# Performance work log

Measured on AMD Instinct MI355X. Metric: run time of the kernel, lower is better.

The kernel has to match this reference:

```python
import jax, jax.numpy as jnp
import numpy as np

B, S = 4, 2048            # batch, seq_len
IN, OUT, NQ = 4096, 4096, 3  # in_features, out_features, num quant levels


def setup_inputs() -> dict:
    key = jax.random.key(0)
    kx, ka = jax.random.split(key, 2)
    x = jax.random.normal(kx, (B, S, IN), dtype=jnp.float32)
    # init_alpha: log(uniform distribution) + tiny noise
    alpha = jnp.log(jnp.full((OUT, IN, NQ), 1.0 / NQ, dtype=jnp.float32)) \
        + 1e-5 * (jax.random.uniform(ka, (OUT, IN, NQ), dtype=jnp.float32) - 0.5)
    quant_vals = jnp.array([-1.0, 0.0, 1.0], dtype=jnp.float32)
    bias = jnp.zeros((OUT,), dtype=jnp.float32)
    return {"x": x, "alpha": alpha, "quant_vals": quant_vals, "bias": bias}


def reference(x, alpha, quant_vals, bias):
    # sample_softmax with temp=1, random=1, hard=False (module globals)
    # gumbels = -log(Exp(1)) == standard Gumbel noise
    g = jax.random.gumbel(jax.random.key(42), alpha.shape, dtype=alpha.dtype)
    y_soft = jax.nn.softmax(alpha + g, axis=-1)          # [OUT, IN, NQ]
    weight = jnp.einsum('oiq,q->oi', y_soft, quant_vals)  # dense dequantized weight
    # F.linear(x, weight, bias) = x @ weight.T + bias
    return jnp.einsum('bsi,oi->bso', x, weight) + bias
```

## Files before the change

### kernel.cpp

```cpp
#include <hip/hip_runtime.h>
#include <hip/hip_fp16.h>
#include <stdint.h>


#define PRNG_PARTITIONABLE 1

#define OUT_F 4096
#define IN_F  4096
#define MROWS 8192
#define NQV   3

typedef __attribute__((ext_vector_type(4))) _Float16 f16x4;
typedef __attribute__((ext_vector_type(8))) _Float16 f16x8;
typedef __attribute__((ext_vector_type(4))) float    f32x4;

__device__ __forceinline__ uint32_t rotl32(uint32_t x, int r) {
  return (x << r) | (x >> (32 - r));
}

__device__ __forceinline__ void threefry2x32(uint32_t x0, uint32_t x1,
                                             uint32_t& o0, uint32_t& o1) {
  const uint32_t ks0 = 0u, ks1 = 42u;
  const uint32_t ks2 = ks0 ^ ks1 ^ 0x1BD11BDAu;
  x0 += ks0; x1 += ks1;
#define TF_R(r) { x0 += x1; x1 = rotl32(x1, r); x1 ^= x0; }
  TF_R(13) TF_R(15) TF_R(26) TF_R(6)
  x0 += ks1; x1 += ks2 + 1u;
  TF_R(17) TF_R(29) TF_R(16) TF_R(24)
  x0 += ks2; x1 += ks0 + 2u;
  TF_R(13) TF_R(15) TF_R(26) TF_R(6)
  x0 += ks0; x1 += ks1 + 3u;
  TF_R(17) TF_R(29) TF_R(16) TF_R(24)
  x0 += ks1; x1 += ks2 + 4u;
  TF_R(13) TF_R(15) TF_R(26) TF_R(6)
  x0 += ks2; x1 += ks0 + 5u;
#undef TF_R
  o0 = x0; o1 = x1;
}

__device__ __forceinline__ uint32_t rand_word(uint32_t e) {
#if PRNG_PARTITIONABLE
  uint32_t o0, o1;
  threefry2x32(0u, e, o0, o1);
  return o0 ^ o1;
#else
  const uint32_t H = (uint32_t)(OUT_F) * IN_F * NQV / 2u;
  uint32_t o0, o1;
  if (e < H) { threefry2x32(e, e + H, o0, o1); return o0; }
  else       { threefry2x32(e - H, e, o0, o1); return o1; }
#endif
}

__device__ __forceinline__ float gumbel_bits(uint32_t bits) {
  float f = __uint_as_float(0x3f800000u | (bits >> 9)) - 1.0f;
  const float tiny = 1.17549435e-38f;
  float u = fmaxf(tiny, f + tiny);
  return -__logf(-__logf(u));
}

__global__ __launch_bounds__(256) void gen_w_kernel(
    const float* __restrict__ alpha, const float* __restrict__ qv,
    _Float16* __restrict__ Wh) {
  int t = blockIdx.x * 256 + threadIdx.x;
  int oi0 = t << 2;
  const float4* ap = (const float4*)(alpha + (size_t)oi0 * 3);
  float4 v0 = ap[0], v1 = ap[1], v2 = ap[2];
  float a[12] = {v0.x, v0.y, v0.z, v0.w, v1.x, v1.y, v1.z, v1.w,
                 v2.x, v2.y, v2.z, v2.w};
  float q0 = qv[0], q1 = qv[1], q2 = qv[2];
  f16x4 wv;
#pragma unroll
  for (int j = 0; j < 4; ++j) {
    uint32_t e = (uint32_t)(oi0 + j) * 3u;
    float s0 = a[3 * j + 0] + gumbel_bits(rand_word(e));
    float s1 = a[3 * j + 1] + gumbel_bits(rand_word(e + 1u));
    float s2 = a[3 * j + 2] + gumbel_bits(rand_word(e + 2u));
    float mx = fmaxf(s0, fmaxf(s1, s2));
    float e0 = __expf(s0 - mx), e1 = __expf(s1 - mx), e2 = __expf(s2 - mx);
    float w = (e0 * q0 + e1 * q1 + e2 * q2) / (e0 + e1 + e2);
    wv[j] = (_Float16)w;
  }
  *(f16x4*)(Wh + oi0) = wv;
}

__global__ __launch_bounds__(256) void cast_x_kernel(
    const float* __restrict__ X, _Float16* __restrict__ Xh) {
  size_t i = ((size_t)blockIdx.x * 256 + threadIdx.x) << 3;
  float4 v0 = *(const float4*)(X + i);
  float4 v1 = *(const float4*)(X + i + 4);
  f16x8 r;
  r[0] = (_Float16)v0.x; r[1] = (_Float16)v0.y;
  r[2] = (_Float16)v0.z; r[3] = (_Float16)v0.w;
  r[4] = (_Float16)v1.x; r[5] = (_Float16)v1.y;
  r[6] = (_Float16)v1.z; r[7] = (_Float16)v1.w;
  *(f16x8*)(Xh + i) = r;
}

#define BM 128
#define BN 128
#define BK 32
#define NTILES_N (OUT_F / BN)

__global__ __launch_bounds__(256) void gemm_kernel(
    const _Float16* __restrict__ X, const _Float16* __restrict__ W,
    const float* __restrict__ bias, float* __restrict__ C) {
  __shared__ __align__(16) _Float16 As[BM * BK];
  __shared__ __align__(16) _Float16 Bs[BN * BK];

  int tid = threadIdx.x;
  int wid = tid >> 6, lane = tid & 63;

  int nwg = gridDim.x;
  int q = nwg >> 3;
  int wg = (blockIdx.x & 7) * q + (blockIdx.x >> 3);
  int mt = wg / NTILES_N, nt = wg % NTILES_N;
  int m0 = mt * BM, n0 = nt * BN;

  int wm = wid >> 1, wn = wid & 1;
  int lr = lane & 15, kg = lane >> 4;

  int aoff[4], boff[4];
#pragma unroll
  for (int f = 0; f < 4; ++f) {
    aoff[f] = (wm * 64 + f * 16 + lr) * BK + kg * 8;
    boff[f] = (wn * 64 + f * 16 + lr) * BK + kg * 8;
  }

  f32x4 acc[4][4] = {};

  int srow0 = tid >> 2, scol0 = (tid & 3) * 8;
  int srow1 = (tid + 256) >> 2, scol1 = ((tid + 256) & 3) * 8;
  int ldsb0 = (wid * 64) * 8;
  int ldsb1 = (256 + wid * 64) * 8;

#define STAGE(k0)                                                             \
  {                                                                           \
    const _Float16* gA0 = X + (size_t)(m0 + srow0) * IN_F + (k0) + scol0;     \
    const _Float16* gB0 = W + (size_t)(n0 + srow0) * IN_F + (k0) + scol0;     \
    const _Float16* gA1 = X + (size_t)(m0 + srow1) * IN_F + (k0) + scol1;     \
    const _Float16* gB1 = W + (size_t)(n0 + srow1) * IN_F + (k0) + scol1;     \
    __builtin_amdgcn_global_load_lds(                                         \
        (const __attribute__((address_space(1))) void*)gA0,                   \
        (__attribute__((address_space(3))) void*)(As + ldsb0), 16, 0, 0);     \
    __builtin_amdgcn_global_load_lds(                                         \
        (const __attribute__((address_space(1))) void*)gB0,                   \
        (__attribute__((address_space(3))) void*)(Bs + ldsb0), 16, 0, 0);     \
    __builtin_amdgcn_global_load_lds(                                         \
        (const __attribute__((address_space(1))) void*)gA1,                   \
        (__attribute__((address_space(3))) void*)(As + ldsb1), 16, 0, 0);     \
    __builtin_amdgcn_global_load_lds(                                         \
        (const __attribute__((address_space(1))) void*)gB1,                   \
        (__attribute__((address_space(3))) void*)(Bs + ldsb1), 16, 0, 0);     \
  }

  STAGE(0)

#pragma unroll 1
  for (int kt = 0; kt < IN_F / BK; ++kt) {
    __syncthreads();
    f16x8 af[4], bf[4];
#pragma unroll
    for (int f = 0; f < 4; ++f) {
      af[f] = *(const f16x8*)(As + aoff[f]);
      bf[f] = *(const f16x8*)(Bs + boff[f]);
    }
#pragma unroll
    for (int i = 0; i < 4; ++i)
#pragma unroll
      for (int j = 0; j < 4; ++j)
        acc[i][j] =
            __builtin_amdgcn_mfma_f32_16x16x32_f16(af[i], bf[j], acc[i][j], 0, 0, 0);
    __syncthreads();
    if (kt + 1 < IN_F / BK) STAGE((kt + 1) * BK)
  }
#undef STAGE

#pragma unroll
  for (int j = 0; j < 4; ++j) {
    int col = n0 + wn * 64 + j * 16 + lr;
    float bv = bias[col];
#pragma unroll
    for (int i = 0; i < 4; ++i) {
      int row0 = m0 + wm * 64 + i * 16 + kg * 4;
#pragma unroll
      for (int r = 0; r < 4; ++r)
        C[(size_t)(row0 + r) * OUT_F + col] = acc[i][j][r] + bv;
    }
  }
}

extern "C" void kernel_launch(void* const* d_in, const int* in_sizes, int n_in,
                              void* d_out, int out_size, void* d_ws,
                              size_t ws_size, hipStream_t stream) {
  const float* x     = (const float*)d_in[0];
  const float* alpha = (const float*)d_in[1];
  const float* qv    = (const float*)d_in[2];
  const float* bias  = (const float*)d_in[3];
  float* out = (float*)d_out;

  _Float16* Wh = (_Float16*)d_ws;
  _Float16* Xh = (_Float16*)((char*)d_ws + (size_t)OUT_F * IN_F * sizeof(_Float16));

  gen_w_kernel<<<dim3((OUT_F * IN_F) / (256 * 4)), dim3(256), 0, stream>>>(alpha, qv, Wh);
  cast_x_kernel<<<dim3(((size_t)MROWS * IN_F) / (256 * 8)), dim3(256), 0, stream>>>(x, Xh);
  gemm_kernel<<<dim3((MROWS / BM) * (OUT_F / BN)), dim3(256), 0, stream>>>(Xh, Wh, bias, out);
}
```

Before: 804.1 us.

## Merge prep kernels and rewrite GEMM with 256x256 tiles and triple-buffered LDS

Merges weight generation and the x cast into a single prep kernel, with alpha staged through shared memory so global loads are coalesced. The GEMM is rewritten to use 256x256 tiles with 8 waves and a three-buffer LDS ring that prefetches two k-steps ahead. It adds XOR swizzling to avoid LDS bank conflicts, split A/B staging interleaved with MFMA phases, and s_setprio around the MFMA blocks. The larger tiles and manual waitcnt/barrier scheduling add register and LDS pressure and raise the risk of synchronisation errors.

Result: faster. 660.7 us (-17.8%).

```diff
diff --git a/kernel.cpp b/kernel.cpp
--- a/kernel.cpp
+++ b/kernel.cpp
@@ -58,133 +58,167 @@
   return -__logf(-__logf(u));
 }
 
-__global__ __launch_bounds__(256) void gen_w_kernel(
+#define GW_BLOCKS 16384
+__global__ __launch_bounds__(256) void prep_kernel(
     const float* __restrict__ alpha, const float* __restrict__ qv,
-    _Float16* __restrict__ Wh) {
-  int t = blockIdx.x * 256 + threadIdx.x;
-  int oi0 = t << 2;
-  const float4* ap = (const float4*)(alpha + (size_t)oi0 * 3);
-  float4 v0 = ap[0], v1 = ap[1], v2 = ap[2];
-  float a[12] = {v0.x, v0.y, v0.z, v0.w, v1.x, v1.y, v1.z, v1.w,
-                 v2.x, v2.y, v2.z, v2.w};
-  float q0 = qv[0], q1 = qv[1], q2 = qv[2];
-  f16x4 wv;
-#pragma unroll
-  for (int j = 0; j < 4; ++j) {
-    uint32_t e = (uint32_t)(oi0 + j) * 3u;
-    float s0 = a[3 * j + 0] + gumbel_bits(rand_word(e));
-    float s1 = a[3 * j + 1] + gumbel_bits(rand_word(e + 1u));
-    float s2 = a[3 * j + 2] + gumbel_bits(rand_word(e + 2u));
-    float mx = fmaxf(s0, fmaxf(s1, s2));
-    float e0 = __expf(s0 - mx), e1 = __expf(s1 - mx), e2 = __expf(s2 - mx);
-    float w = (e0 * q0 + e1 * q1 + e2 * q2) / (e0 + e1 + e2);
-    wv[j] = (_Float16)w;
+    const float* __restrict__ X, _Float16* __restrict__ Wh,
+    _Float16* __restrict__ Xh) {
+  __shared__ float sb[3072];
+  int tid = threadIdx.x;
+  int blk = blockIdx.x;
+  if (blk < GW_BLOCKS) {
+    const float4* g = (const float4*)(alpha + (size_t)blk * 3072);
+    float4 v0 = g[tid], v1 = g[tid + 256], v2 = g[tid + 512];
+    float4* s4 = (float4*)sb;
+    s4[tid] = v0; s4[tid + 256] = v1; s4[tid + 512] = v2;
+    __syncthreads();
+    const float4* rp = (const float4*)(sb + tid * 12);
+    float4 a0 = rp[0], a1 = rp[1], a2 = rp[2];
+    float a[12] = {a0.x, a0.y, a0.z, a0.w, a1.x, a1.y, a1.z, a1.w,
+                   a2.x, a2.y, a2.z, a2.w};
+    float q0 = qv[0], q1 = qv[1], q2 = qv[2];
+    int oi0 = blk * 1024 + tid * 4;
+    uint32_t ebase = (uint32_t)blk * 3072u + (uint32_t)tid * 12u;
+    f16x4 wv;
+#pragma unroll
+    for (int j = 0; j < 4; ++j) {
+      uint32_t e = ebase + (uint32_t)(3 * j);
+      float s0 = a[3 * j + 0] + gumbel_bits(rand_word(e));
+      float s1 = a[3 * j + 1] + gumbel_bits(rand_word(e + 1u));
+      float s2 = a[3 * j + 2] + gumbel_bits(rand_word(e + 2u));
+      float mx = fmaxf(s0, fmaxf(s1, s2));
+      float e0 = __expf(s0 - mx), e1 = __expf(s1 - mx), e2 = __expf(s2 - mx);
+      float w = (e0 * q0 + e1 * q1 + e2 * q2) / (e0 + e1 + e2);
+      wv[j] = (_Float16)w;
+    }
+    *(f16x4*)(Wh + oi0) = wv;
+  } else {
+    size_t i = (((size_t)(blk - GW_BLOCKS)) * 256 + tid) << 3;
+    float4 v0 = *(const float4*)(X + i);
+    float4 v1 = *(const float4*)(X + i + 4);
+    f16x8 r;
+    r[0] = (_Float16)v0.x; r[1] = (_Float16)v0.y;
+    r[2] = (_Float16)v0.z; r[3] = (_Float16)v0.w;
+    r[4] = (_Float16)v1.x; r[5] = (_Float16)v1.y;
+    r[6] = (_Float16)v1.z; r[7] = (_Float16)v1.w;
+    *(f16x8*)(Xh + i) = r;
   }
-  *(f16x4*)(Wh + oi0) = wv;
-}
-
-__global__ __launch_bounds__(256) void cast_x_kernel(
-    const float* __restrict__ X, _Float16* __restrict__ Xh) {
-  size_t i = ((size_t)blockIdx.x * 256 + threadIdx.x) << 3;
-  float4 v0 = *(const float4*)(X + i);
-  float4 v1 = *(const float4*)(X + i + 4);
-  f16x8 r;
-  r[0] = (_Float16)v0.x; r[1] = (_Float16)v0.y;
-  r[2] = (_Float16)v0.z; r[3] = (_Float16)v0.w;
-  r[4] = (_Float16)v1.x; r[5] = (_Float16)v1.y;
-  r[6] = (_Float16)v1.z; r[7] = (_Float16)v1.w;
-  *(f16x8*)(Xh + i) = r;
-}
-
-#define BM 128
-#define BN 128
-#define BK 32
-#define NTILES_N (OUT_F / BN)
-
-__global__ __launch_bounds__(256) void gemm_kernel(
+}
+
+#define NT 128
+
+__global__ __launch_bounds__(512, 2) void gemm_kernel(
     const _Float16* __restrict__ X, const _Float16* __restrict__ W,
     const float* __restrict__ bias, float* __restrict__ C) {
-  __shared__ __align__(16) _Float16 As[BM * BK];
-  __shared__ __align__(16) _Float16 Bs[BN * BK];
+  __shared__ __align__(16) _Float16 lds[49152];
 
   int tid = threadIdx.x;
   int wid = tid >> 6, lane = tid & 63;
-
-  int nwg = gridDim.x;
-  int q = nwg >> 3;
-  int wg = (blockIdx.x & 7) * q + (blockIdx.x >> 3);
-  int mt = wg / NTILES_N, nt = wg % NTILES_N;
-  int m0 = mt * BM, n0 = nt * BN;
-
-  int wm = wid >> 1, wn = wid & 1;
   int lr = lane & 15, kg = lane >> 4;
-
-  int aoff[4], boff[4];
-#pragma unroll
-  for (int f = 0; f < 4; ++f) {
-    aoff[f] = (wm * 64 + f * 16 + lr) * BK + kg * 8;
-    boff[f] = (wn * 64 + f * 16 + lr) * BK + kg * 8;
+  int wm = wid >> 2, wn = wid & 3;
+
+  int bid = blockIdx.x;
+  int wg = (bid & 7) * 64 + (bid >> 3);
+  int mt = wg >> 4, nt = wg & 15;
+  int m0 = mt * 256, n0 = nt * 256;
+
+  int s0 = tid, s1 = 512 + tid;
+  int r0row = s0 >> 2, r0kb = (s0 & 3) ^ ((r0row >> 1) & 3);
+  int r1row = s1 >> 2, r1kb = (s1 & 3) ^ ((r1row >> 1) & 3);
+  int dst0 = (wid * 64) * 8;
+  int dst1 = (512 + wid * 64) * 8;
+
+  const _Float16* Xb = X + (size_t)m0 * IN_F;
+  const _Float16* Wb = W + (size_t)n0 * IN_F;
+
+#define GLD(src, dstp)                                                        \
+  __builtin_amdgcn_global_load_lds(                                           \
+      (const __attribute__((address_space(1))) void*)(src),                   \
+      (__attribute__((address_space(3))) void*)(dstp), 16, 0, 0)
+
+#define STAGE_A(t, bufp) {                                                    \
+    GLD(Xb + (size_t)r0row * IN_F + (t) * 32 + r0kb * 8, (bufp) + dst0);      \
+    GLD(Xb + (size_t)r1row * IN_F + (t) * 32 + r1kb * 8, (bufp) + dst1); }
+#define STAGE_B(t, bufp) {                                                    \
+    GLD(Wb + (size_t)r0row * IN_F + (t) * 32 + r0kb * 8, (bufp) + 8192 + dst0);\
+    GLD(Wb + (size_t)r1row * IN_F + (t) * 32 + r1kb * 8, (bufp) + 8192 + dst1); }
+
+  f32x4 acc[8][4] = {};
+  int koff = (kg ^ ((lr >> 1) & 3)) * 8;
+
+  STAGE_A(0, lds); STAGE_B(0, lds);
+  STAGE_A(1, lds + 16384); STAGE_B(1, lds + 16384);
+  asm volatile("s_waitcnt vmcnt(4)" ::: "memory");
+  __builtin_amdgcn_s_barrier();
+
+  int buf = 0;
+#pragma unroll 1
+  for (int t = 0; t < NT; ++t) {
+    _Float16* Ab = lds + buf * 16384;
+    _Float16* Bb = Ab + 8192;
+    int nbuf = buf + 2; if (nbuf >= 3) nbuf -= 3;
+    _Float16* Nb = lds + nbuf * 16384;
+
+    f16x8 af[4], bf[4];
+#pragma unroll
+    for (int f = 0; f < 4; ++f)
+      af[f] = *(const f16x8*)(Ab + (wm * 128 + f * 16 + lr) * 32 + koff);
+#pragma unroll
+    for (int g = 0; g < 4; ++g)
+      bf[g] = *(const f16x8*)(Bb + (wn * 64 + g * 16 + lr) * 32 + koff);
+    if (t + 2 < NT) STAGE_A(t + 2, Nb);
+    __builtin_amdgcn_s_barrier();
+    asm volatile("s_waitcnt lgkmcnt(0)" ::: "memory");
+    __builtin_amdgcn_sched_barrier(0);
+    __builtin_amdgcn_s_setprio(1);
+#pragma unroll
+    for (int f = 0; f < 4; ++f)
+#pragma unroll
+      for (int g = 0; g < 4; ++g)
+        acc[f][g] = __builtin_amdgcn_mfma_f32_16x16x32_f16(af[f], bf[g],
+                                                           acc[f][g], 0, 0, 0);
+    __builtin_amdgcn_s_setprio(0);
+    __builtin_amdgcn_s_barrier();
+
+#pragma unroll
+    for (int f = 0; f < 4; ++f)
+      af[f] = *(const f16x8*)(Ab + (wm * 128 + 64 + f * 16 + lr) * 32 + koff);
+    if (t + 2 < NT) {
+      STAGE_B(t + 2, Nb);
+      asm volatile("s_waitcnt vmcnt(4)" ::: "memory");
+    } else if (t < NT - 1) {
+      asm volatile("s_waitcnt vmcnt(0)" ::: "memory");
+    }
+    __builtin_amdgcn_s_barrier();
+    asm volatile("s_waitcnt lgkmcnt(0)" ::: "memory");
+    __builtin_amdgcn_sched_barrier(0);
+    __builtin_amdgcn_s_setprio(1);
+#pragma unroll
+    for (int f = 0; f < 4; ++f)
+#pragma unroll
+      for (int g = 0; g < 4; ++g)
+        acc[4 + f][g] = __builtin_amdgcn_mfma_f32_16x16x32_f16(af[f], bf[g],
+                                                               acc[4 + f][g],
+                                                               0, 0, 0);
+    __builtin_amdgcn_s_setprio(0);
+    __builtin_amdgcn_s_barrier();
+
+    buf = (buf + 1 == 3) ? 0 : buf + 1;
   }
-
-  f32x4 acc[4][4] = {};
-
-  int srow0 = tid >> 2, scol0 = (tid & 3) * 8;
-  int srow1 = (tid + 256) >> 2, scol1 = ((tid + 256) & 3) * 8;
-  int ldsb0 = (wid * 64) * 8;
-  int ldsb1 = (256 + wid * 64) * 8;
-
-#define STAGE(k0)                                                             \
-  {                                                                           \
-    const _Float16* gA0 = X + (size_t)(m0 + srow0) * IN_F + (k0) + scol0;     \
-    const _Float16* gB0 = W + (size_t)(n0 + srow0) * IN_F + (k0) + scol0;     \
-    const _Float16* gA1 = X + (size_t)(m0 + srow1) * IN_F + (k0) + scol1;     \
-    const _Float16* gB1 = W + (size_t)(n0 + srow1) * IN_F + (k0) + scol1;     \
-    __builtin_amdgcn_global_load_lds(                                         \
-        (const __attribute__((address_space(1))) void*)gA0,                   \
-        (__attribute__((address_space(3))) void*)(As + ldsb0), 16, 0, 0);     \
-    __builtin_amdgcn_global_load_lds(                                         \
-        (const __attribute__((address_space(1))) void*)gB0,                   \
-        (__attribute__((address_space(3))) void*)(Bs + ldsb0), 16, 0, 0);     \
-    __builtin_amdgcn_global_load_lds(                                         \
-        (const __attribute__((address_space(1))) void*)gA1,                   \
-        (__attribute__((address_space(3))) void*)(As + ldsb1), 16, 0, 0);     \
-    __builtin_amdgcn_global_load_lds(                                         \
-        (const __attribute__((address_space(1))) void*)gB1,                   \
-        (__attribute__((address_space(3))) void*)(Bs + ldsb1), 16, 0, 0);     \
-  }
-
-  STAGE(0)
-
-#pragma unroll 1
-  for (int kt = 0; kt < IN_F / BK; ++kt) {
-    __syncthreads();
-    f16x8 af[4], bf[4];
-#pragma unroll
-    for (int f = 0; f < 4; ++f) {
-      af[f] = *(const f16x8*)(As + aoff[f]);
-      bf[f] = *(const f16x8*)(Bs + boff[f]);
-    }
-#pragma unroll
-    for (int i = 0; i < 4; ++i)
-#pragma unroll
-      for (int j = 0; j < 4; ++j)
-        acc[i][j] =
-            __builtin_amdgcn_mfma_f32_16x16x32_f16(af[i], bf[j], acc[i][j], 0, 0, 0);
-    __syncthreads();
-    if (kt + 1 < IN_F / BK) STAGE((kt + 1) * BK)
-  }
-#undef STAGE
-
-#pragma unroll
-  for (int j = 0; j < 4; ++j) {
-    int col = n0 + wn * 64 + j * 16 + lr;
+#undef STAGE_A
+#undef STAGE_B
+#undef GLD
+
+#pragma unroll
+  for (int g = 0; g < 4; ++g) {
+    int col = n0 + wn * 64 + g * 16 + lr;
     float bv = bias[col];
 #pragma unroll
-    for (int i = 0; i < 4; ++i) {
-      int row0 = m0 + wm * 64 + i * 16 + kg * 4;
+    for (int f = 0; f < 8; ++f) {
+      int row0 = m0 + wm * 128 + f * 16 + kg * 4;
 #pragma unroll
       for (int r = 0; r < 4; ++r)
-        C[(size_t)(row0 + r) * OUT_F + col] = acc[i][j][r] + bv;
+        C[(size_t)(row0 + r) * OUT_F + col] = acc[f][g][r] + bv;
     }
   }
 }
@@ -201,7 +235,7 @@
   _Float16* Wh = (_Float16*)d_ws;
   _Float16* Xh = (_Float16*)((char*)d_ws + (size_t)OUT_F * IN_F * sizeof(_Float16));
 
-  gen_w_kernel<<<dim3((OUT_F * IN_F) / (256 * 4)), dim3(256), 0, stream>>>(alpha, qv, Wh);
-  cast_x_kernel<<<dim3(((size_t)MROWS * IN_F) / (256 * 8)), dim3(256), 0, stream>>>(x, Xh);
-  gemm_kernel<<<dim3((MROWS / BM) * (OUT_F / BN)), dim3(256), 0, stream>>>(Xh, Wh, bias, out);
-}
+  prep_kernel<<<dim3(32768), dim3(256), 0, stream>>>(alpha, qv, x, Wh, Xh);
+  gemm_kernel<<<dim3((MROWS / 256) * (OUT_F / 256)), dim3(512), 0, stream>>>(
+      Xh, Wh, bias, out);
+}
```
